# Kernel tuning notes

Hardware: AMD Instinct MI355X
Metric: run time of the kernel (lower is better)

Reference implementation:

```python
import jax, jax.numpy as jnp
import numpy as np

D_MODEL = 1024
NUM_HEADS = 16
HEAD_DIM = D_MODEL // NUM_HEADS
THETA = 10000.0
B, S = 1, 2048


def setup_inputs() -> dict:
    key = jax.random.key(0)
    ks = jax.random.split(key, 7)
    sc = 0.02
    return {
        "query": jax.random.normal(ks[0], (B, S, D_MODEL), jnp.float32),
        "key": jax.random.normal(ks[1], (B, S, D_MODEL), jnp.float32),
        "value": jax.random.normal(ks[2], (B, S, D_MODEL), jnp.float32),
        "qkv_w": jax.random.normal(ks[3], (3 * D_MODEL, D_MODEL), jnp.float32) * sc,
        "qkv_b": jax.random.normal(ks[4], (3 * D_MODEL,), jnp.float32) * sc,
        "out_w": jax.random.normal(ks[5], (D_MODEL, D_MODEL), jnp.float32) * sc,
        "out_b": jax.random.normal(ks[6], (D_MODEL,), jnp.float32) * sc,
    }


def _rope_cos_sin(seq_len, head_dim, dtype):
    # freqs_for='lang': inv_freq = theta^(-2i/d), i = 0..d/2-1
    inv_freq = 1.0 / (THETA ** (jnp.arange(0, head_dim, 2, dtype=jnp.float32) / head_dim))
    t = jnp.arange(seq_len, dtype=jnp.float32)
    freqs = jnp.outer(t, inv_freq)                      # [S, d/2]
    emb = jnp.concatenate([freqs, freqs], axis=-1)      # [S, d] (non-interleaved)
    return jnp.cos(emb).astype(dtype), jnp.sin(emb).astype(dtype)


def _rotate_half(x):
    half = x.shape[-1] // 2
    return jnp.concatenate([-x[..., half:], x[..., :half]], axis=-1)


def reference(query, key, value, qkv_w, qkv_b, out_w, out_b):
    # NOTE: module computes q,k,v all from `query` (key/value args unused).
    b, s, d = query.shape
    qkv = query @ qkv_w.T + qkv_b                       # [B,S,3D]
    qkv = qkv.reshape(b, s, 3, NUM_HEADS, HEAD_DIM)
    qkv = jnp.transpose(qkv, (2, 0, 3, 1, 4))           # [3,B,H,S,hd]
    q, k, v = qkv[0], qkv[1], qkv[2]

    cos, sin = _rope_cos_sin(s, HEAD_DIM, query.dtype)  # [S,hd]
    q = q * cos + _rotate_half(q) * sin
    k = k * cos + _rotate_half(k) * sin

    scale = 1.0 / np.sqrt(HEAD_DIM)
    scores = jnp.einsum('bhqd,bhkd->bhqk', q, k) * scale
    attn = jax.nn.softmax(scores, axis=-1)
    ctx = jnp.einsum('bhqk,bhkd->bhqd', attn, v)        # [B,H,S,hd]
    ctx = jnp.transpose(ctx, (0, 2, 1, 3)).reshape(b, s, d)
    return ctx @ out_w.T + out_b
```

## Files before the change

kernel.cpp:

```cpp
#include <hip/hip_runtime.h>
#include <math.h>
#include <stdint.h>

#define SEQ 2048
#define DM  1024
#define NH  16
#define HD  64
#define TRI 3072
#define NSPLIT 4

typedef _Float16 half8 __attribute__((ext_vector_type(8)));
typedef __fp16 fp16x2 __attribute__((ext_vector_type(2)));
typedef float f32x4 __attribute__((ext_vector_type(4)));

#define GLOAD_LDS16(g, l)                                       \
  __builtin_amdgcn_global_load_lds(                             \
      (__attribute__((address_space(1))) void*)(g),             \
      (__attribute__((address_space(3))) void*)(l), 16, 0, 0)

#define QSCALE 0.18033688011112042f

__global__ __launch_bounds__(256)
void cvt3(const float* __restrict__ s1, const float* __restrict__ s2,
          const float* __restrict__ s3, _Float16* __restrict__ d1,
          _Float16* __restrict__ d2, _Float16* __restrict__ d3,
          float2* __restrict__ tab, int n1, int n2) {
  int b = blockIdx.x;
  if (b >= 6144) {
    int i = (b - 6144) * 256 + threadIdx.x;
    int s = i >> 5, d = i & 31;
    float inv = exp2f((float)d * -0.4152410118609203f);
    float ang = (float)s * inv;
    float sn, cs;
    sincosf(ang, &sn, &cs);
    tab[i] = make_float2(cs, sn);
    return;
  }
  int i = (b * 256 + threadIdx.x) * 4;
  const float* s; _Float16* d;
  if (i < n1)            { s = s1; d = d1; }
  else if (i < n1 + n2)  { s = s2; d = d2; i -= n1; }
  else                   { s = s3; d = d3; i -= n1 + n2; }
  float4 v = *(const float4*)(s + i);
  union { _Float16 h[4]; uint2 u; } pk;
  pk.h[0] = (_Float16)v.x; pk.h[1] = (_Float16)v.y;
  pk.h[2] = (_Float16)v.z; pk.h[3] = (_Float16)v.w;
  *(uint2*)(d + i) = pk.u;
}

template<int EPI, typename OutT>
__global__ __launch_bounds__(256)
void gemm_p3(const _Float16* __restrict__ A, const _Float16* __restrict__ B,
             const float* __restrict__ bias, const float2* __restrict__ tab,
             OutT* __restrict__ C, _Float16* __restrict__ Ko,
             _Float16* __restrict__ Vo, int N) {
  constexpr int K = DM;
  __shared__ _Float16 As[3][64 * 32];
  __shared__ _Float16 Bs[3][128 * 32];

  const int t = threadIdx.x, lane = t & 63, wv = t >> 6;
  const int l15 = lane & 15, l4 = lane >> 4;
  const int wr = wv >> 1, wc = wv & 1;
  const int bm = blockIdx.y * 64, bn = blockIdx.x * 128;

  auto stage = [&](int buf, int k0) {
    {
      int c = t;
      GLOAD_LDS16(A + (size_t)(bm + (c >> 2)) * K + k0 + (c & 3) * 8,
                  (char*)&As[buf][wv * 512]);
    }
    #pragma unroll
    for (int i = 0; i < 2; ++i) {
      int c = t + i * 256;
      GLOAD_LDS16(B + (size_t)(bn + (c >> 2)) * K + k0 + (c & 3) * 8,
                  (char*)&Bs[buf][(i * 256 + wv * 64) * 8]);
    }
  };

  f32x4 acc[2][4] = {};
  stage(0, 0);
  stage(1, 32);

  const int nk = K / 32;
  for (int s = 0; s < nk; ++s) {
    int cur = s % 3;
    if (s + 1 < nk) asm volatile("s_waitcnt vmcnt(3)" ::: "memory");
    else            asm volatile("s_waitcnt vmcnt(0)" ::: "memory");
    __builtin_amdgcn_s_barrier();
    __builtin_amdgcn_sched_barrier(0);
    if (s + 2 < nk) stage((s + 2) % 3, (s + 2) * 32);

    half8 af[2], bf[4];
    #pragma unroll
    for (int mf = 0; mf < 2; ++mf)
      af[mf] = *(const half8*)&As[cur][(wr * 32 + mf * 16 + l15) * 32 + l4 * 8];
    #pragma unroll
    for (int nf = 0; nf < 4; ++nf)
      bf[nf] = *(const half8*)&Bs[cur][(wc * 64 + nf * 16 + l15) * 32 + l4 * 8];
    __builtin_amdgcn_s_setprio(1);
    #pragma unroll
    for (int mf = 0; mf < 2; ++mf)
      #pragma unroll
      for (int nf = 0; nf < 4; ++nf)
        acc[mf][nf] = __builtin_amdgcn_mfma_f32_16x16x32_f16(
            af[mf], bf[nf], acc[mf][nf], 0, 0, 0);
    __builtin_amdgcn_s_setprio(0);
  }

  float bv[4];
  #pragma unroll
  for (int nf = 0; nf < 4; ++nf) bv[nf] = bias[bn + wc * 64 + nf * 16 + l15];

  if (EPI == 0) {
    #pragma unroll
    for (int mf = 0; mf < 2; ++mf)
      #pragma unroll
      for (int r = 0; r < 4; ++r) {
        int row = bm + wr * 32 + mf * 16 + l4 * 4 + r;
        OutT* cr = C + (size_t)row * N + bn + wc * 64 + l15;
        cr[0]  = (OutT)(acc[mf][0][r] + bv[0]);
        cr[16] = (OutT)(acc[mf][1][r] + bv[1]);
        cr[32] = (OutT)(acc[mf][2][r] + bv[2]);
        cr[48] = (OutT)(acc[mf][3][r] + bv[3]);
      }
    return;
  }

  const int sec = bn >> 10;
  if (sec < 2) {
    OutT* dst = (sec == 0) ? C : (OutT*)Ko;
    #pragma unroll
    for (int mf = 0; mf < 2; ++mf)
      #pragma unroll
      for (int r = 0; r < 4; ++r) {
        int row = bm + wr * 32 + mf * 16 + l4 * 4 + r;
        float v0 = acc[mf][0][r] + bv[0];
        float v1 = acc[mf][1][r] + bv[1];
        float v2 = acc[mf][2][r] + bv[2];
        float v3 = acc[mf][3][r] + bv[3];
        float2 cs0 = tab[row * 32 + l15];
        float2 cs1 = tab[row * 32 + 16 + l15];
        float a0 = v0 * cs0.x - v2 * cs0.y;
        float a2 = v2 * cs0.x + v0 * cs0.y;
        float a1 = v1 * cs1.x - v3 * cs1.y;
        float a3 = v3 * cs1.x + v1 * cs1.y;
        if (sec == 0) { a0 *= QSCALE; a1 *= QSCALE; a2 *= QSCALE; a3 *= QSCALE; }
        OutT* cr = dst + (size_t)row * DM + (bn & 1023) + wc * 64 + l15;
        cr[0]  = (OutT)a0; cr[16] = (OutT)a1;
        cr[32] = (OutT)a2; cr[48] = (OutT)a3;
      }
  } else {
    const int hh = ((bn - 2048) >> 6) + wc;
    #pragma unroll
    for (int mf = 0; mf < 2; ++mf) {
      int row0 = bm + wr * 32 + mf * 16 + l4 * 4;
      int kk0 = row0 & 63, kseg = row0 >> 6;
      #pragma unroll
      for (int nf = 0; nf < 4; ++nf) {
        int d = nf * 16 + l15;
        union { _Float16 hh4[4]; uint2 u; } pk;
        #pragma unroll
        for (int r = 0; r < 4; ++r)
          pk.hh4[r] = (_Float16)(acc[mf][nf][r] + bv[nf]);
        size_t off = ((size_t)(hh * 32 + kseg) * 64 + d) * 64 +
                     (((kk0 >> 3) ^ (d & 7)) * 8) + (kk0 & 7);
        *(uint2*)(Vo + off) = pk.u;
      }
    }
  }
}

__global__ __launch_bounds__(256)
void attn_f16(const _Float16* __restrict__ Qg, const _Float16* __restrict__ Kg,
              const _Float16* __restrict__ Vg, _Float16* __restrict__ poA,
              _Float16* __restrict__ po3, float* __restrict__ pl) {
  __shared__ _Float16 Kl[2][64 * 64];
  __shared__ _Float16 Vt[2][64 * 64];

  const int t = threadIdx.x, lane = t & 63, wv = t >> 6;
  const int l15 = lane & 15, l4 = lane >> 4;
  const int bid = blockIdx.x;
  const int c = bid & 63, qb = bid >> 6;
  const int h = c & 15, z = c >> 4;
  const int q0 = qb * 64;
  const int seg0 = z * (SEQ / NSPLIT / 64);

  const _Float16* Qp = Qg + h * HD;
  const _Float16* Kp = Kg + h * HD;
  const _Float16* Vbase = Vg + (size_t)h * 32 * 4096;

  half8 qf[2];
  {
    const _Float16* qrow = Qp + (size_t)(q0 + wv * 16 + l15) * DM;
    qf[0] = *(const half8*)(qrow + l4 * 8);
    qf[1] = *(const half8*)(qrow + 32 + l4 * 8);
  }

  int koff[2];
  #pragma unroll
  for (int i = 0; i < 2; ++i) {
    int cc = t + i * 256, kk = cc >> 3, p = cc & 7;
    int hkk = (kk & 3) | ((kk >> 1) & 4);
    koff[i] = kk * DM + ((p ^ hkk) * 8);
  }

  auto issueKV = [&](int buf, int seg) {
    const _Float16* ks = Kp + (size_t)seg * 64 * DM;
    const _Float16* vs = Vbase + (size_t)seg * 4096;
    GLOAD_LDS16(ks + koff[0],               (char*)&Kl[buf][(wv * 64) * 8]);
    GLOAD_LDS16(ks + koff[1],               (char*)&Kl[buf][(256 + wv * 64) * 8]);
    GLOAD_LDS16(vs + (size_t)t * 8,         (char*)&Vt[buf][(wv * 64) * 8]);
    GLOAD_LDS16(vs + (size_t)(t + 256) * 8, (char*)&Vt[buf][(256 + wv * 64) * 8]);
  };

  f32x4 lacc = {0.f, 0.f, 0.f, 0.f};
  f32x4 o[4] = {};

  const int hk = (l15 & 3) | (((l15 >> 2) & 1) << 2);
  const int krow = 8 * (l15 >> 2) + (l15 & 3);

  issueKV(0, seg0);

  const int NT = SEQ / NSPLIT / 64;
  #pragma unroll 2
  for (int tt = 0; tt < NT; ++tt) {
    const int cur = tt & 1;
    asm volatile("s_waitcnt vmcnt(0)" ::: "memory");
    __builtin_amdgcn_s_barrier();
    __builtin_amdgcn_sched_barrier(0);
    if (tt + 1 < NT) issueKV(cur ^ 1, seg0 + tt + 1);

    f32x4 sT[4] = {};
    __builtin_amdgcn_s_setprio(1);
    #pragma unroll
    for (int ds = 0; ds < 2; ++ds)
      #pragma unroll
      for (int m = 0; m < 4; ++m) {
        int kappa = 32 * (m >> 1) + 4 * (m & 1) + krow;
        int cb = ds * 4 + l4;
        half8 kf = *(const half8*)((char*)Kl[cur] + kappa * 128 +
                                   ((cb ^ hk) * 16));
        sT[m] = __builtin_amdgcn_mfma_f32_16x16x32_f16(kf, qf[ds], sT[m], 0, 0, 0);
      }
    __builtin_amdgcn_s_setprio(0);

    half8 pB[2];
    #pragma unroll
    for (int s2 = 0; s2 < 2; ++s2) {
      union { fp16x2 h2[4]; half8 v; } pu;
      #pragma unroll
      for (int mh = 0; mh < 2; ++mh) {
        int m = s2 * 2 + mh;
        f32x4 p;
        #pragma unroll
        for (int r = 0; r < 4; ++r) p[r] = exp2f(sT[m][r]);
        lacc += p;
        pu.h2[mh * 2 + 0] = __builtin_amdgcn_cvt_pkrtz(p[0], p[1]);
        pu.h2[mh * 2 + 1] = __builtin_amdgcn_cvt_pkrtz(p[2], p[3]);
      }
      pB[s2] = pu.v;
    }

    __builtin_amdgcn_s_setprio(1);
    #pragma unroll
    for (int s2 = 0; s2 < 2; ++s2)
      #pragma unroll
      for (int nf = 0; nf < 4; ++nf) {
        half8 va = *(const half8*)((char*)Vt[cur] + (nf * 16 + l15) * 128 +
                                   (((s2 * 4 + l4) ^ (l15 & 7)) * 16));
        o[nf] = __builtin_amdgcn_mfma_f32_16x16x32_f16(va, pB[s2], o[nf], 0, 0, 0);
      }
    __builtin_amdgcn_s_setprio(0);
  }

  float lv = (lacc[0] + lacc[1]) + (lacc[2] + lacc[3]);
  lv += __shfl_xor(lv, 16);
  lv += __shfl_xor(lv, 32);
  _Float16* pz = (z < 3) ? (poA + (size_t)z * SEQ * DM) : po3;
  {
    int row = q0 + wv * 16 + l15;
    _Float16* pr = pz + (size_t)row * DM + h * HD + l4 * 4;
    #pragma unroll
    for (int nf = 0; nf < 4; ++nf) {
      union { fp16x2 h2[2]; uint2 u; } ou;
      ou.h2[0] = __builtin_amdgcn_cvt_pkrtz(o[nf][0], o[nf][1]);
      ou.h2[1] = __builtin_amdgcn_cvt_pkrtz(o[nf][2], o[nf][3]);
      *(uint2*)(pr + nf * 16) = ou.u;
    }
  }
  if (l4 == 0) {
    int q = q0 + wv * 16 + l15;
    pl[(z * NH + h) * SEQ + q] = lv;
  }
}

__global__ __launch_bounds__(256)
void merge4(const _Float16* __restrict__ poA, const _Float16* __restrict__ po3,
            const float* __restrict__ pl, _Float16* __restrict__ ctx) {
  int e = (blockIdx.x * 256 + threadIdx.x) * 8;
  int s = e >> 10, h = (e & 1023) >> 6;
  int idx = h * SEQ + s;
  float L = pl[idx] + pl[NH * SEQ + idx] + pl[2 * NH * SEQ + idx] +
            pl[3 * NH * SEQ + idx];
  float inv = 1.0f / L;
  half8 a = *(const half8*)(poA + e);
  half8 b = *(const half8*)(poA + (size_t)SEQ * DM + e);
  half8 cc = *(const half8*)(poA + 2 * (size_t)SEQ * DM + e);
  half8 d = *(const half8*)(po3 + e);
  half8 o;
  #pragma unroll
  for (int j = 0; j < 8; ++j)
    o[j] = (_Float16)((((float)a[j] + (float)b[j]) +
                       ((float)cc[j] + (float)d[j])) * inv);
  *(half8*)(ctx + e) = o;
}

extern "C" void kernel_launch(void* const* d_in, const int* in_sizes, int n_in,
                              void* d_out, int out_size, void* d_ws, size_t ws_size,
                              hipStream_t stream) {
  const float* query = (const float*)d_in[0];
  const float* qkv_w = (const float*)d_in[3];
  const float* qkv_b = (const float*)d_in[4];
  const float* out_w = (const float*)d_in[5];
  const float* out_b = (const float*)d_in[6];
  float* out = (float*)d_out;

  char* ws = (char*)d_ws;
  _Float16* Aq   = (_Float16*)ws;
  _Float16* Wqkv = (_Float16*)(ws + (4u << 20));
  _Float16* Qb   = (_Float16*)(ws + (12u << 20));
  _Float16* Kb   = (_Float16*)(ws + (16u << 20));
  _Float16* Vb   = (_Float16*)(ws + (20u << 20));
  _Float16* ctx  = (_Float16*)(ws + (24u << 20));
  float2*   tab  = (float2*)(ws + (28u << 20));
  _Float16* Wout = (_Float16*)(ws + (28u << 20) + (512u << 10));
  float*    pl   = (float*)(ws + (30u << 20) + (512u << 10));
  _Float16* poA  = (_Float16*)ws;
  _Float16* po3  = ctx;

  cvt3<<<6400, 256, 0, stream>>>(query, qkv_w, out_w, Aq, Wqkv, Wout, tab,
                                 SEQ * DM, TRI * DM);

  gemm_p3<1, _Float16><<<dim3(TRI / 128, SEQ / 64), 256, 0, stream>>>(
      Aq, Wqkv, qkv_b, tab, Qb, Kb, Vb, TRI);

  attn_f16<<<(SEQ / 64) * NH * NSPLIT, 256, 0, stream>>>(
      Qb, Kb, Vb, poA, po3, pl);

  merge4<<<SEQ * DM / 8 / 256, 256, 0, stream>>>(poA, po3, pl, ctx);

  gemm_p3<0, float><<<dim3(DM / 128, SEQ / 64), 256, 0, stream>>>(
      ctx, Wout, out_b, nullptr, out, nullptr, nullptr, DM);
}
```

Measured before the change: 93.85 us.

## Enlarge QKV GEMM row tile and attention query block to share K/V tiles

The GEMM kernel is templated on its row-tile height. The QKV projection now uses 128-row tiles, with extra A-tile loads per stage and a matching vmcnt wait, while the output projection stays at 64 rows. The attention kernel moves to 512 threads covering 128 query rows per block, so each staged K/V tile is shared by eight waves instead of four and every thread issues half as many loads. This cuts redundant global and LDS traffic, but it shrinks the grids (fewer, larger blocks), which can leave CUs idle or lower occupancy.

```diff
diff --git a/kernel.cpp b/kernel.cpp
--- a/kernel.cpp
+++ b/kernel.cpp
@@ -48,26 +48,30 @@
   *(uint2*)(d + i) = pk.u;
 }
 
-template<int EPI, typename OutT>
+template<int BM, int EPI, typename OutT>
 __global__ __launch_bounds__(256)
 void gemm_p3(const _Float16* __restrict__ A, const _Float16* __restrict__ B,
              const float* __restrict__ bias, const float2* __restrict__ tab,
              OutT* __restrict__ C, _Float16* __restrict__ Ko,
              _Float16* __restrict__ Vo, int N) {
   constexpr int K = DM;
-  __shared__ _Float16 As[3][64 * 32];
+  constexpr int MFR = BM / 32;
+  constexpr int ACH = BM * 4 / 256;
+  constexpr int NOPS = ACH + 2;
+  __shared__ _Float16 As[3][BM * 32];
   __shared__ _Float16 Bs[3][128 * 32];
 
   const int t = threadIdx.x, lane = t & 63, wv = t >> 6;
   const int l15 = lane & 15, l4 = lane >> 4;
   const int wr = wv >> 1, wc = wv & 1;
-  const int bm = blockIdx.y * 64, bn = blockIdx.x * 128;
+  const int bm = blockIdx.y * BM, bn = blockIdx.x * 128;
 
   auto stage = [&](int buf, int k0) {
-    {
-      int c = t;
+    #pragma unroll
+    for (int i = 0; i < ACH; ++i) {
+      int c = t + i * 256;
       GLOAD_LDS16(A + (size_t)(bm + (c >> 2)) * K + k0 + (c & 3) * 8,
-                  (char*)&As[buf][wv * 512]);
+                  (char*)&As[buf][(i * 256 + wv * 64) * 8]);
     }
     #pragma unroll
     for (int i = 0; i < 2; ++i) {
@@ -77,29 +81,33 @@
     }
   };
 
-  f32x4 acc[2][4] = {};
+  f32x4 acc[MFR][4] = {};
   stage(0, 0);
   stage(1, 32);
 
   const int nk = K / 32;
   for (int s = 0; s < nk; ++s) {
     int cur = s % 3;
-    if (s + 1 < nk) asm volatile("s_waitcnt vmcnt(3)" ::: "memory");
-    else            asm volatile("s_waitcnt vmcnt(0)" ::: "memory");
+    if (s + 1 < nk) {
+      if constexpr (NOPS == 3) asm volatile("s_waitcnt vmcnt(3)" ::: "memory");
+      else                     asm volatile("s_waitcnt vmcnt(4)" ::: "memory");
+    } else {
+      asm volatile("s_waitcnt vmcnt(0)" ::: "memory");
+    }
     __builtin_amdgcn_s_barrier();
     __builtin_amdgcn_sched_barrier(0);
     if (s + 2 < nk) stage((s + 2) % 3, (s + 2) * 32);
 
-    half8 af[2], bf[4];
-    #pragma unroll
-    for (int mf = 0; mf < 2; ++mf)
-      af[mf] = *(const half8*)&As[cur][(wr * 32 + mf * 16 + l15) * 32 + l4 * 8];
+    half8 af[MFR], bf[4];
+    #pragma unroll
+    for (int mf = 0; mf < MFR; ++mf)
+      af[mf] = *(const half8*)&As[cur][(wr * (BM / 2) + mf * 16 + l15) * 32 + l4 * 8];
     #pragma unroll
     for (int nf = 0; nf < 4; ++nf)
       bf[nf] = *(const half8*)&Bs[cur][(wc * 64 + nf * 16 + l15) * 32 + l4 * 8];
     __builtin_amdgcn_s_setprio(1);
     #pragma unroll
-    for (int mf = 0; mf < 2; ++mf)
+    for (int mf = 0; mf < MFR; ++mf)
       #pragma unroll
       for (int nf = 0; nf < 4; ++nf)
         acc[mf][nf] = __builtin_amdgcn_mfma_f32_16x16x32_f16(
@@ -113,10 +121,10 @@
 
   if (EPI == 0) {
     #pragma unroll
-    for (int mf = 0; mf < 2; ++mf)
+    for (int mf = 0; mf < MFR; ++mf)
       #pragma unroll
       for (int r = 0; r < 4; ++r) {
-        int row = bm + wr * 32 + mf * 16 + l4 * 4 + r;
+        int row = bm + wr * (BM / 2) + mf * 16 + l4 * 4 + r;
         OutT* cr = C + (size_t)row * N + bn + wc * 64 + l15;
         cr[0]  = (OutT)(acc[mf][0][r] + bv[0]);
         cr[16] = (OutT)(acc[mf][1][r] + bv[1]);
@@ -130,10 +138,10 @@
   if (sec < 2) {
     OutT* dst = (sec == 0) ? C : (OutT*)Ko;
     #pragma unroll
-    for (int mf = 0; mf < 2; ++mf)
+    for (int mf = 0; mf < MFR; ++mf)
       #pragma unroll
       for (int r = 0; r < 4; ++r) {
-        int row = bm + wr * 32 + mf * 16 + l4 * 4 + r;
+        int row = bm + wr * (BM / 2) + mf * 16 + l4 * 4 + r;
         float v0 = acc[mf][0][r] + bv[0];
         float v1 = acc[mf][1][r] + bv[1];
         float v2 = acc[mf][2][r] + bv[2];
@@ -152,8 +160,8 @@
   } else {
     const int hh = ((bn - 2048) >> 6) + wc;
     #pragma unroll
-    for (int mf = 0; mf < 2; ++mf) {
-      int row0 = bm + wr * 32 + mf * 16 + l4 * 4;
+    for (int mf = 0; mf < MFR; ++mf) {
+      int row0 = bm + wr * (BM / 2) + mf * 16 + l4 * 4;
       int kk0 = row0 & 63, kseg = row0 >> 6;
       #pragma unroll
       for (int nf = 0; nf < 4; ++nf) {
@@ -170,7 +178,7 @@
   }
 }
 
-__global__ __launch_bounds__(256)
+__global__ __launch_bounds__(512)
 void attn_f16(const _Float16* __restrict__ Qg, const _Float16* __restrict__ Kg,
               const _Float16* __restrict__ Vg, _Float16* __restrict__ poA,
               _Float16* __restrict__ po3, float* __restrict__ pl) {
@@ -182,7 +190,7 @@
   const int bid = blockIdx.x;
   const int c = bid & 63, qb = bid >> 6;
   const int h = c & 15, z = c >> 4;
-  const int q0 = qb * 64;
+  const int q0 = qb * 128;
   const int seg0 = z * (SEQ / NSPLIT / 64);
 
   const _Float16* Qp = Qg + h * HD;
@@ -196,21 +204,18 @@
     qf[1] = *(const half8*)(qrow + 32 + l4 * 8);
   }
 
-  int koff[2];
-  #pragma unroll
-  for (int i = 0; i < 2; ++i) {
-    int cc = t + i * 256, kk = cc >> 3, p = cc & 7;
+  int koff;
+  {
+    int kk = t >> 3, p = t & 7;
     int hkk = (kk & 3) | ((kk >> 1) & 4);
-    koff[i] = kk * DM + ((p ^ hkk) * 8);
+    koff = kk * DM + ((p ^ hkk) * 8);
   }
 
   auto issueKV = [&](int buf, int seg) {
     const _Float16* ks = Kp + (size_t)seg * 64 * DM;
     const _Float16* vs = Vbase + (size_t)seg * 4096;
-    GLOAD_LDS16(ks + koff[0],               (char*)&Kl[buf][(wv * 64) * 8]);
-    GLOAD_LDS16(ks + koff[1],               (char*)&Kl[buf][(256 + wv * 64) * 8]);
-    GLOAD_LDS16(vs + (size_t)t * 8,         (char*)&Vt[buf][(wv * 64) * 8]);
-    GLOAD_LDS16(vs + (size_t)(t + 256) * 8, (char*)&Vt[buf][(256 + wv * 64) * 8]);
+    GLOAD_LDS16(ks + koff,          (char*)&Kl[buf][(wv * 64) * 8]);
+    GLOAD_LDS16(vs + (size_t)t * 8, (char*)&Vt[buf][(wv * 64) * 8]);
   };
 
   f32x4 lacc = {0.f, 0.f, 0.f, 0.f};
@@ -341,14 +346,14 @@
   cvt3<<<6400, 256, 0, stream>>>(query, qkv_w, out_w, Aq, Wqkv, Wout, tab,
                                  SEQ * DM, TRI * DM);
 
-  gemm_p3<1, _Float16><<<dim3(TRI / 128, SEQ / 64), 256, 0, stream>>>(
+  gemm_p3<128, 1, _Float16><<<dim3(TRI / 128, SEQ / 128), 256, 0, stream>>>(
       Aq, Wqkv, qkv_b, tab, Qb, Kb, Vb, TRI);
 
-  attn_f16<<<(SEQ / 64) * NH * NSPLIT, 256, 0, stream>>>(
+  attn_f16<<<(SEQ / 128) * NH * NSPLIT, 512, 0, stream>>>(
       Qb, Kb, Vb, poA, po3, pl);
 
   merge4<<<SEQ * DM / 8 / 256, 256, 0, stream>>>(poA, po3, pl, ctx);
 
-  gemm_p3<0, float><<<dim3(DM / 128, SEQ / 64), 256, 0, stream>>>(
+  gemm_p3<64, 0, float><<<dim3(DM / 128, SEQ / 64), 256, 0, stream>>>(
       ctx, Wout, out_b, nullptr, out, nullptr, nullptr, DM);
 }
```

After: 92.72 us (median of 2 runs). Within noise of the previous version (-1.2%).
